# Kernel tuning notes

Hardware: AMD Instinct MI355X
Metric: run time of the kernel (lower is better)

Reference implementation:

```python
import jax, jax.numpy as jnp
import numpy as np

N = 4096
IN_DIM = 256
HID = 64
NHEADS = 4
OUT_DIM = 128
ALPHA = 0.5  # LeakyReLU negative slope
NEG_INF = -9e15


def gat_layer(x, mask, W, a, concat):
    """Dense GraphAttentionLayer (pyGAT style).
    x:[N,Fin], mask:[N,N] bool, W:[Fin,Fout], a:[2*Fout]."""
    Wh = x @ W                                   # [N, Fout]
    Fout = W.shape[1]
    f1 = Wh @ a[:Fout]                           # [N]
    f2 = Wh @ a[Fout:]                           # [N]
    e = jax.nn.leaky_relu(f1[:, None] + f2[None, :], negative_slope=ALPHA)  # [N,N]
    att = jax.nn.softmax(jnp.where(mask, e, NEG_INF), axis=1)               # [N,N]
    h = att @ Wh                                 # [N, Fout]
    return jax.nn.elu(h) if concat else h


def setup_inputs() -> dict:
    key = jax.random.key(0)
    ks = jax.random.split(key, 6)
    x = jax.random.normal(ks[0], (N, IN_DIM), dtype=jnp.float32)
    adj = jax.random.randint(ks[1], (N, N), 0, 2, dtype=jnp.int32)
    s_in = 1.0 / np.sqrt(IN_DIM)
    s_hid = 1.0 / np.sqrt(HID * NHEADS)
    W_heads = jax.random.uniform(ks[2], (NHEADS, IN_DIM, HID), jnp.float32, -s_in, s_in)
    a_heads = jax.random.uniform(ks[3], (NHEADS, 2 * HID), jnp.float32, -s_in, s_in)
    W_out = jax.random.uniform(ks[4], (HID * NHEADS, OUT_DIM), jnp.float32, -s_hid, s_hid)
    a_out = jax.random.uniform(ks[5], (2 * OUT_DIM,), jnp.float32, -s_hid, s_hid)
    return {"x": x, "adj": adj, "W_heads": W_heads, "a_heads": a_heads,
            "W_out": W_out, "a_out": a_out}


def reference(x, adj, W_heads, a_heads, W_out, a_out):
    mask = adj > 0
    # multi-head attention, concat along feature dim
    heads = jax.vmap(lambda W, a: gat_layer(x, mask, W, a, True))(W_heads, a_heads)
    h = jnp.transpose(heads, (1, 0, 2)).reshape(N, NHEADS * HID)  # [N, H*HID]
    # dropout=0 -> identity; final GAT layer (concat=False) + outer ELU
    out = jax.nn.elu(gat_layer(h, mask, W_out, a_out, False))     # [N, OUT_DIM]
    return out
```

## Files before the change

### kernel.cpp

```cpp
#include <hip/hip_runtime.h>
#include <hip/hip_bf16.h>

#define N 4096
#define IN_DIM 256
#define HID 64
#define NHEADS 4
#define OUT_DIM 128
#define LOG2E 1.44269504088896340736f

typedef __attribute__((ext_vector_type(8))) short bf16x8;
typedef __attribute__((ext_vector_type(4))) float f32x4;

__device__ __forceinline__ ushort2 bsplit(float v) {
    const ushort h = __hip_bfloat16_raw(__float2bfloat16(v)).x;
    const float vh = __uint_as_float((unsigned)h << 16);
    const ushort l = __hip_bfloat16_raw(__float2bfloat16(v - vh)).x;
    return make_ushort2(h, l);
}

__global__ __launch_bounds__(256, 4) void prep_kernel(
        const float* __restrict__ x, const float* __restrict__ W,
        const float* __restrict__ a, const int* __restrict__ adj,
        __hip_bfloat16* __restrict__ WhB,
        float* __restrict__ f1, float* __restrict__ f2,
        unsigned* __restrict__ maskT) {
    const int t = threadIdx.x;
    if (blockIdx.x < 256) {
        const int h = t >> 6, lane = t & 63, m = lane & 15, quad = lane >> 4;
        const int i0 = blockIdx.x * 16;
        const float* xrow = x + (size_t)(i0 + m) * IN_DIM;
        const float* Wp = W + (size_t)h * IN_DIM * HID;
        const f32x4 zero = {0.f, 0.f, 0.f, 0.f};
        f32x4 acc[4] = {zero, zero, zero, zero};
        for (int ks = 0; ks < 8; ks++) {
            const int kb = ks * 32 + quad * 8;
            const float4 xa = *(const float4*)(xrow + kb);
            const float4 xb = *(const float4*)(xrow + kb + 4);
            const float xf[8] = {xa.x, xa.y, xa.z, xa.w, xb.x, xb.y, xb.z, xb.w};
            bf16x8 xh, xl;
#pragma unroll
            for (int e = 0; e < 8; e++) {
                const ushort2 s = bsplit(xf[e]);
                xh[e] = (short)s.x; xl[e] = (short)s.y;
            }
#pragma unroll
            for (int ct = 0; ct < 4; ct++) {
                bf16x8 wh, wl;
#pragma unroll
                for (int e = 0; e < 8; e++) {
                    const ushort2 s =
                        bsplit(Wp[(size_t)(kb + e) * HID + ct * 16 + m]);
                    wh[e] = (short)s.x; wl[e] = (short)s.y;
                }
                acc[ct] = __builtin_amdgcn_mfma_f32_16x16x32_bf16(
                    xh, wh, acc[ct], 0, 0, 0);
                acc[ct] = __builtin_amdgcn_mfma_f32_16x16x32_bf16(
                    xl, wh, acc[ct], 0, 0, 0);
                acc[ct] = __builtin_amdgcn_mfma_f32_16x16x32_bf16(
                    xh, wl, acc[ct], 0, 0, 0);
            }
        }
        const int jblk = i0 >> 5, jb2 = (i0 >> 4) & 1;
#pragma unroll
        for (int ct = 0; ct < 4; ct++) {
#pragma unroll
            for (int r = 0; r < 4; r++) {
                const int jo = quad * 4 + r;
                const int lane_idx = m + 16 * (2 * jb2 + (jo >> 3));
                WhB[((((size_t)h * (N / 32) + jblk) * 4 + ct) * 64 + lane_idx) *
                        8 + (jo & 7)] = __float2bfloat16(acc[ct][r]);
            }
        }
        float av1[4], av2[4];
#pragma unroll
        for (int ct = 0; ct < 4; ct++) {
            av1[ct] = a[h * 2 * HID + ct * 16 + m];
            av2[ct] = a[h * 2 * HID + HID + ct * 16 + m];
        }
        float s1[4], s2[4];
#pragma unroll
        for (int r = 0; r < 4; r++) {
            s1[r] = 0.f; s2[r] = 0.f;
#pragma unroll
            for (int ct = 0; ct < 4; ct++) {
                s1[r] += acc[ct][r] * av1[ct];
                s2[r] += acc[ct][r] * av2[ct];
            }
        }
#pragma unroll
        for (int mm = 8; mm > 0; mm >>= 1) {
#pragma unroll
            for (int r = 0; r < 4; r++) {
                s1[r] += __shfl_xor(s1[r], mm, 64);
                s2[r] += __shfl_xor(s2[r], mm, 64);
            }
        }
        if (m == 0) {
#pragma unroll
            for (int r = 0; r < 4; r++) {
                f1[(size_t)h * N + i0 + quad * 4 + r] = s1[r] * LOG2E;
                f2[(size_t)h * N + i0 + quad * 4 + r] = s2[r] * LOG2E;
            }
        }
    } else {
        const int lane = t & 63, w = t >> 6;
        const int i = (blockIdx.x - 256) * 4 + w;
        const int4* arow = (const int4*)(adj + (size_t)i * N);
        for (int jb = 0; jb < N / 256; jb++) {
            const int4 a4 = arow[jb * 64 + lane];
            unsigned long long bal[4];
            bal[0] = __ballot(a4.x > 0);
            bal[1] = __ballot(a4.y > 0);
            bal[2] = __ballot(a4.z > 0);
            bal[3] = __ballot(a4.w > 0);
            if (lane < 8) {
                unsigned word = 0;
#pragma unroll
                for (int e = 0; e < 4; e++) {
                    unsigned xv = (unsigned)(bal[e] >> (8 * lane)) & 0xFFu;
                    xv = (xv | (xv << 12)) & 0x000F000Fu;
                    xv = (xv | (xv << 6))  & 0x03030303u;
                    xv = (xv | (xv << 3))  & 0x11111111u;
                    word |= xv << e;
                }
                maskT[(size_t)(jb * 8 + lane) * N + i] = word;
            }
        }
    }
}

template <int HEADS, int D, int DSL, int G, int MW, int OCC>
__global__ __launch_bounds__(G * 64, OCC) void attn_fused(
        const unsigned* __restrict__ maskT,
        const __hip_bfloat16* __restrict__ WhB,
        const float* __restrict__ f1g, const float* __restrict__ f2g,
        float* __restrict__ outp) {
    constexpr int CTtot = D / 16;
    constexpr int CTT = CTtot / DSL;
    constexpr int CC = (D == 64) ? 1 : 2;
    constexpr int KSTEPS = N / (32 * G);
    __shared__ float sh[MW * G * 16 * CC * 17];
    __shared__ float dsh[MW * G * 16];
    const int t = threadIdx.x;
    const int g = t >> 6, lane = t & 63;
    const int m = lane & 15, quad = lane >> 4;
    const int h = blockIdx.y / DSL, slc = blockIdx.y % DSL;
    const int i0 = blockIdx.x * (16 * MW);

    float f1v[MW];
#pragma unroll
    for (int mw = 0; mw < MW; mw++)
        f1v[mw] = f1g[(size_t)h * N + i0 + mw * 16 + m];

    const unsigned* mp = maskT + (size_t)(g * KSTEPS) * N + i0 + m;
    const float* fp = f2g + (size_t)h * N + g * (N / G) + quad * 8;
    const bf16x8* bp = (const bf16x8*)WhB +
                       ((size_t)h * (N / 32) * CTtot +
                        (size_t)(g * KSTEPS) * CTtot + slc * CTT) * 64 + lane;

    const f32x4 zero = {0.f, 0.f, 0.f, 0.f};
    f32x4 acc[MW][CTT];
    f32x4 sac[MW];
#pragma unroll
    for (int mw = 0; mw < MW; mw++) {
        sac[mw] = zero;
#pragma unroll
        for (int ct = 0; ct < CTT; ct++) acc[mw][ct] = zero;
    }
    const short one_bf = (short)0x3F80;
    const bf16x8 ones = {one_bf, one_bf, one_bf, one_bf,
                         one_bf, one_bf, one_bf, one_bf};

    unsigned mwrd[2][MW];
    float4 f2lo[2], f2hi[2];
    auto stage = [&](int b) {
#pragma unroll
        for (int mw = 0; mw < MW; mw++) mwrd[b][mw] = mp[mw * 16];
        f2lo[b] = *(const float4*)(fp);
        f2hi[b] = *(const float4*)(fp + 4);
    };

    stage(0); mp += N; fp += 32;
#pragma unroll 2
    for (int ks = 0; ks < KSTEPS; ks++) {
        const int cur = ks & 1;
        bf16x8 bfrag[CTT];
#pragma unroll
        for (int ct = 0; ct < CTT; ct++) bfrag[ct] = bp[ct * 64];
        bp += CTtot * 64;
        if (ks + 1 < KSTEPS) { stage(cur ^ 1); mp += N; fp += 32; }
        const float fe[8] = {f2lo[cur].x, f2lo[cur].y, f2lo[cur].z, f2lo[cur].w,
                             f2hi[cur].x, f2hi[cur].y, f2hi[cur].z, f2hi[cur].w};
        bf16x8 afr[MW];
#pragma unroll
        for (int mw = 0; mw < MW; mw++) {
            const unsigned mword = (mwrd[cur][mw] >> (quad * 8)) & 0xFFu;
            const unsigned spread = mword * 0x8001u;
            float p[8];
#pragma unroll
            for (int e = 0; e < 8; e++) {
                const float tt = f1v[mw] + fe[e];
                const float lr = fmaxf(tt, 0.5f * tt);
                p[e] = __builtin_amdgcn_exp2f(lr);
            }
            union { bf16x8 v; unsigned u32[4]; __hip_bfloat162 h2[4]; } u;
#pragma unroll
            for (int e2 = 0; e2 < 4; e2++) {
                u.h2[e2] = __float22bfloat162_rn(
                    make_float2(p[2 * e2], p[2 * e2 + 1]));
                const unsigned mk =
                    ((spread >> (2 * e2)) & 0x00010001u) * 0xFFFFu;
                u.u32[e2] &= mk;
            }
            afr[mw] = u.v;
        }
#pragma unroll
        for (int ct = 0; ct < CTT; ct++)
#pragma unroll
            for (int mw = 0; mw < MW; mw++)
                acc[mw][ct] = __builtin_amdgcn_mfma_f32_16x16x32_bf16(
                    afr[mw], bfrag[ct], acc[mw][ct], 0, 0, 0);
#pragma unroll
        for (int mw = 0; mw < MW; mw++)
            sac[mw] = __builtin_amdgcn_mfma_f32_16x16x32_bf16(
                afr[mw], ones, sac[mw], 0, 0, 0);
    }

#pragma unroll
    for (int rd = 0; rd < CTT / CC; rd++) {
#pragma unroll
        for (int mw = 0; mw < MW; mw++) {
#pragma unroll
            for (int cc = 0; cc < CC; cc++) {
#pragma unroll
                for (int r = 0; r < 4; r++)
                    sh[(((mw * G + g) * 16 + quad * 4 + r) * CC + cc) * 17 + m] =
                        acc[mw][rd * CC + cc][r];
            }
            if (rd == 0 && m == 0) {
#pragma unroll
                for (int r = 0; r < 4; r++)
                    dsh[(mw * G + g) * 16 + quad * 4 + r] = sac[mw][r];
            }
        }
        __syncthreads();
        if (t < 16 * CC * 16) {
            int row, chl;
            if (D == 64) { row = t & 15; chl = (t >> 4) & 15; }
            else         { chl = t & 31; row = (t >> 5) & 15; }
#pragma unroll
            for (int mw = 0; mw < MW; mw++) {
                float av = 0.f, ss = 0.f;
#pragma unroll
                for (int gg = 0; gg < G; gg++) {
                    av += sh[(((mw * G + gg) * 16 + row) * CC + (chl >> 4)) * 17 +
                             (chl & 15)];
                    ss += dsh[(mw * G + gg) * 16 + row];
                }
                float v = av / ss;
                v = (v > 0.f) ? v : (__builtin_amdgcn_exp2f(v * LOG2E) - 1.f);
                const int chg = h * D + slc * (CTT * 16) + rd * CC * 16 + chl;
                const int irow = i0 + mw * 16 + row;
                if (D == 64)
                    outp[(size_t)irow * (NHEADS * HID) + chg] = v;
                else
                    outp[(size_t)irow * D + chg] = v;
            }
        }
        __syncthreads();
    }
}

__global__ __launch_bounds__(512, 2) void gemm2_kernel(
        const float* __restrict__ h1, const float* __restrict__ W2,
        const float* __restrict__ a2, __hip_bfloat16* __restrict__ WhB2,
        float* __restrict__ f1, float* __restrict__ f2) {
    __shared__ float fred[8][16][2];
    const int t = threadIdx.x;
    const int w = t >> 6, lane = t & 63, m = lane & 15, quad = lane >> 4;
    const int i0 = blockIdx.x * 16;
    const float* arow = h1 + (size_t)(i0 + m) * IN_DIM;
    const float* wp = W2 + w * 16 + m;
    const f32x4 zero = {0.f, 0.f, 0.f, 0.f};
    f32x4 acc = zero;
    for (int ks = 0; ks < 8; ks++) {
        const int kb = ks * 32 + quad * 8;
        const float4 xa = *(const float4*)(arow + kb);
        const float4 xb = *(const float4*)(arow + kb + 4);
        const float xf[8] = {xa.x, xa.y, xa.z, xa.w, xb.x, xb.y, xb.z, xb.w};
        bf16x8 xh, xl, wh, wl;
#pragma unroll
        for (int e = 0; e < 8; e++) {
            const ushort2 s = bsplit(xf[e]);
            xh[e] = (short)s.x; xl[e] = (short)s.y;
        }
#pragma unroll
        for (int e = 0; e < 8; e++) {
            const ushort2 s = bsplit(wp[(size_t)(kb + e) * OUT_DIM]);
            wh[e] = (short)s.x; wl[e] = (short)s.y;
        }
        acc = __builtin_amdgcn_mfma_f32_16x16x32_bf16(xh, wh, acc, 0, 0, 0);
        acc = __builtin_amdgcn_mfma_f32_16x16x32_bf16(xl, wh, acc, 0, 0, 0);
        acc = __builtin_amdgcn_mfma_f32_16x16x32_bf16(xh, wl, acc, 0, 0, 0);
    }
    const int jblk = i0 >> 5, jb2 = (i0 >> 4) & 1;
#pragma unroll
    for (int r = 0; r < 4; r++) {
        const int jo = quad * 4 + r;
        const int lane_idx = m + 16 * (2 * jb2 + (jo >> 3));
        WhB2[(((size_t)jblk * 8 + w) * 64 + lane_idx) * 8 + (jo & 7)] =
            __float2bfloat16(acc[r]);
    }
    const float av1 = a2[w * 16 + m], av2 = a2[OUT_DIM + w * 16 + m];
    float s1[4], s2[4];
#pragma unroll
    for (int r = 0; r < 4; r++) { s1[r] = acc[r] * av1; s2[r] = acc[r] * av2; }
#pragma unroll
    for (int mm = 8; mm > 0; mm >>= 1) {
#pragma unroll
        for (int r = 0; r < 4; r++) {
            s1[r] += __shfl_xor(s1[r], mm, 64);
            s2[r] += __shfl_xor(s2[r], mm, 64);
        }
    }
    if (m == 0) {
#pragma unroll
        for (int r = 0; r < 4; r++) {
            fred[w][quad * 4 + r][0] = s1[r];
            fred[w][quad * 4 + r][1] = s2[r];
        }
    }
    __syncthreads();
    if (t < 32) {
        const int row = t & 15, fn = t >> 4;
        float s = 0.f;
#pragma unroll
        for (int w8 = 0; w8 < 8; w8++) s += fred[w8][row][fn];
        (fn ? f2 : f1)[i0 + row] = s * LOG2E;
    }
}

extern "C" void kernel_launch(void* const* d_in, const int* in_sizes, int n_in,
                              void* d_out, int out_size, void* d_ws, size_t ws_size,
                              hipStream_t stream) {
    const float* x   = (const float*)d_in[0];
    const int*   adj = (const int*)d_in[1];
    const float* Wh_ = (const float*)d_in[2];
    const float* ah  = (const float*)d_in[3];
    const float* W2  = (const float*)d_in[4];
    const float* a2  = (const float*)d_in[5];
    float* out = (float*)d_out;

    float* ws = (float*)d_ws;
    float* f1a = ws;
    float* f2a = f1a + (size_t)NHEADS * N;
    float* f1b = f2a + (size_t)NHEADS * N;
    float* f2b = f1b + N;
    float* h1  = f2b + N;
    __hip_bfloat16* WhB1 = (__hip_bfloat16*)(h1 + (size_t)IN_DIM * N);
    __hip_bfloat16* WhB2 = WhB1 + (size_t)NHEADS * HID * N;
    unsigned* maskT = (unsigned*)(WhB2 + (size_t)OUT_DIM * N);

    prep_kernel<<<1280, 256, 0, stream>>>(x, Wh_, ah, adj, WhB1, f1a, f2a, maskT);
    attn_fused<NHEADS, HID, 1, 8, 1, 8>
        <<<dim3(N / 16, NHEADS), 512, 0, stream>>>(maskT, WhB1, f1a, f2a, h1);
    gemm2_kernel<<<N / 16, 512, 0, stream>>>(h1, W2, a2, WhB2, f1b, f2b);
    attn_fused<1, OUT_DIM, 1, 16, 1, 4>
        <<<dim3(N / 16, 1), 1024, 0, stream>>>(maskT, WhB2, f1b, f2b, out);
}
```

Before: 191.1 us.

## Factor exp of leaky-relu scores into per-node products, retune attention launches

```diff
diff --git a/kernel.cpp b/kernel.cpp
--- a/kernel.cpp
+++ b/kernel.cpp
@@ -22,7 +22,8 @@
         const float* __restrict__ x, const float* __restrict__ W,
         const float* __restrict__ a, const int* __restrict__ adj,
         __hip_bfloat16* __restrict__ WhB,
-        float* __restrict__ f1, float* __restrict__ f2,
+        float* __restrict__ E1, float* __restrict__ S1,
+        float* __restrict__ E2, float* __restrict__ S2,
         unsigned* __restrict__ maskT) {
     const int t = threadIdx.x;
     if (blockIdx.x < 256) {
@@ -98,8 +99,11 @@
         if (m == 0) {
 #pragma unroll
             for (int r = 0; r < 4; r++) {
-                f1[(size_t)h * N + i0 + quad * 4 + r] = s1[r] * LOG2E;
-                f2[(size_t)h * N + i0 + quad * 4 + r] = s2[r] * LOG2E;
+                const size_t ix = (size_t)h * N + i0 + quad * 4 + r;
+                E1[ix] = __builtin_amdgcn_exp2f(s1[r] * LOG2E);
+                S1[ix] = __builtin_amdgcn_exp2f(s1[r] * (0.5f * LOG2E));
+                E2[ix] = __builtin_amdgcn_exp2f(s2[r] * LOG2E);
+                S2[ix] = __builtin_amdgcn_exp2f(s2[r] * (0.5f * LOG2E));
             }
         }
     } else {
@@ -133,7 +137,8 @@
 __global__ __launch_bounds__(G * 64, OCC) void attn_fused(
         const unsigned* __restrict__ maskT,
         const __hip_bfloat16* __restrict__ WhB,
-        const float* __restrict__ f1g, const float* __restrict__ f2g,
+        const float* __restrict__ E1g, const float* __restrict__ S1g,
+        const float* __restrict__ E2g, const float* __restrict__ S2g,
         float* __restrict__ outp) {
     constexpr int CTtot = D / 16;
     constexpr int CTT = CTtot / DSL;
@@ -147,13 +152,16 @@
     const int h = blockIdx.y / DSL, slc = blockIdx.y % DSL;
     const int i0 = blockIdx.x * (16 * MW);
 
-    float f1v[MW];
-#pragma unroll
-    for (int mw = 0; mw < MW; mw++)
-        f1v[mw] = f1g[(size_t)h * N + i0 + mw * 16 + m];
+    float e1v[MW], s1v[MW];
+#pragma unroll
+    for (int mw = 0; mw < MW; mw++) {
+        e1v[mw] = E1g[(size_t)h * N + i0 + mw * 16 + m];
+        s1v[mw] = S1g[(size_t)h * N + i0 + mw * 16 + m];
+    }
 
     const unsigned* mp = maskT + (size_t)(g * KSTEPS) * N + i0 + m;
-    const float* fp = f2g + (size_t)h * N + g * (N / G) + quad * 8;
+    const float* ep = E2g + (size_t)h * N + g * (N / G) + quad * 8;
+    const float* sp = S2g + (size_t)h * N + g * (N / G) + quad * 8;
     const bf16x8* bp = (const bf16x8*)WhB +
                        ((size_t)h * (N / 32) * CTtot +
                         (size_t)(g * KSTEPS) * CTtot + slc * CTT) * 64 + lane;
@@ -172,15 +180,17 @@
                          one_bf, one_bf, one_bf, one_bf};
 
     unsigned mwrd[2][MW];
-    float4 f2lo[2], f2hi[2];
+    float4 e2lo[2], e2hi[2], s2lo[2], s2hi[2];
     auto stage = [&](int b) {
 #pragma unroll
         for (int mw = 0; mw < MW; mw++) mwrd[b][mw] = mp[mw * 16];
-        f2lo[b] = *(const float4*)(fp);
-        f2hi[b] = *(const float4*)(fp + 4);
+        e2lo[b] = *(const float4*)(ep);
+        e2hi[b] = *(const float4*)(ep + 4);
+        s2lo[b] = *(const float4*)(sp);
+        s2hi[b] = *(const float4*)(sp + 4);
     };
 
-    stage(0); mp += N; fp += 32;
+    stage(0); mp += N; ep += 32; sp += 32;
 #pragma unroll 2
     for (int ks = 0; ks < KSTEPS; ks++) {
         const int cur = ks & 1;
@@ -188,9 +198,11 @@
 #pragma unroll
         for (int ct = 0; ct < CTT; ct++) bfrag[ct] = bp[ct * 64];
         bp += CTtot * 64;
-        if (ks + 1 < KSTEPS) { stage(cur ^ 1); mp += N; fp += 32; }
-        const float fe[8] = {f2lo[cur].x, f2lo[cur].y, f2lo[cur].z, f2lo[cur].w,
-                             f2hi[cur].x, f2hi[cur].y, f2hi[cur].z, f2hi[cur].w};
+        if (ks + 1 < KSTEPS) { stage(cur ^ 1); mp += N; ep += 32; sp += 32; }
+        const float Ee[8] = {e2lo[cur].x, e2lo[cur].y, e2lo[cur].z, e2lo[cur].w,
+                             e2hi[cur].x, e2hi[cur].y, e2hi[cur].z, e2hi[cur].w};
+        const float Se[8] = {s2lo[cur].x, s2lo[cur].y, s2lo[cur].z, s2lo[cur].w,
+                             s2hi[cur].x, s2hi[cur].y, s2hi[cur].z, s2hi[cur].w};
         bf16x8 afr[MW];
 #pragma unroll
         for (int mw = 0; mw < MW; mw++) {
@@ -198,11 +210,8 @@
             const unsigned spread = mword * 0x8001u;
             float p[8];
 #pragma unroll
-            for (int e = 0; e < 8; e++) {
-                const float tt = f1v[mw] + fe[e];
-                const float lr = fmaxf(tt, 0.5f * tt);
-                p[e] = __builtin_amdgcn_exp2f(lr);
-            }
+            for (int e = 0; e < 8; e++)
+                p[e] = fmaxf(e1v[mw] * Ee[e], s1v[mw] * Se[e]);
             union { bf16x8 v; unsigned u32[4]; __hip_bfloat162 h2[4]; } u;
 #pragma unroll
             for (int e2 = 0; e2 < 4; e2++) {
@@ -274,7 +283,8 @@
 __global__ __launch_bounds__(512, 2) void gemm2_kernel(
         const float* __restrict__ h1, const float* __restrict__ W2,
         const float* __restrict__ a2, __hip_bfloat16* __restrict__ WhB2,
-        float* __restrict__ f1, float* __restrict__ f2) {
+        float* __restrict__ E1, float* __restrict__ S1,
+        float* __restrict__ E2, float* __restrict__ S2) {
     __shared__ float fred[8][16][2];
     const int t = threadIdx.x;
     const int w = t >> 6, lane = t & 63, m = lane & 15, quad = lane >> 4;
@@ -336,7 +346,10 @@
         float s = 0.f;
 #pragma unroll
         for (int w8 = 0; w8 < 8; w8++) s += fred[w8][row][fn];
-        (fn ? f2 : f1)[i0 + row] = s * LOG2E;
+        const float e = __builtin_amdgcn_exp2f(s * LOG2E);
+        const float sq = __builtin_amdgcn_exp2f(s * (0.5f * LOG2E));
+        if (fn) { E2[i0 + row] = e; S2[i0 + row] = sq; }
+        else    { E1[i0 + row] = e; S1[i0 + row] = sq; }
     }
 }
 
@@ -352,19 +365,27 @@
     float* out = (float*)d_out;
 
     float* ws = (float*)d_ws;
-    float* f1a = ws;
-    float* f2a = f1a + (size_t)NHEADS * N;
-    float* f1b = f2a + (size_t)NHEADS * N;
-    float* f2b = f1b + N;
-    float* h1  = f2b + N;
+    float* E1a = ws;
+    float* S1a = E1a + (size_t)NHEADS * N;
+    float* E2a = S1a + (size_t)NHEADS * N;
+    float* S2a = E2a + (size_t)NHEADS * N;
+    float* E1b = S2a + (size_t)NHEADS * N;
+    float* S1b = E1b + N;
+    float* E2b = S1b + N;
+    float* S2b = E2b + N;
+    float* h1  = S2b + N;
     __hip_bfloat16* WhB1 = (__hip_bfloat16*)(h1 + (size_t)IN_DIM * N);
     __hip_bfloat16* WhB2 = WhB1 + (size_t)NHEADS * HID * N;
     unsigned* maskT = (unsigned*)(WhB2 + (size_t)OUT_DIM * N);
 
-    prep_kernel<<<1280, 256, 0, stream>>>(x, Wh_, ah, adj, WhB1, f1a, f2a, maskT);
-    attn_fused<NHEADS, HID, 1, 8, 1, 8>
-        <<<dim3(N / 16, NHEADS), 512, 0, stream>>>(maskT, WhB1, f1a, f2a, h1);
-    gemm2_kernel<<<N / 16, 512, 0, stream>>>(h1, W2, a2, WhB2, f1b, f2b);
-    attn_fused<1, OUT_DIM, 1, 16, 1, 4>
-        <<<dim3(N / 16, 1), 1024, 0, stream>>>(maskT, WhB2, f1b, f2b, out);
-}
+    prep_kernel<<<1280, 256, 0, stream>>>(x, Wh_, ah, adj, WhB1,
+                                          E1a, S1a, E2a, S2a, maskT);
+    attn_fused<NHEADS, HID, 1, 8, 2, 2>
+        <<<dim3(N / 32, NHEADS), 512, 0, stream>>>(maskT, WhB1,
+                                                   E1a, S1a, E2a, S2a, h1);
+    gemm2_kernel<<<N / 16, 512, 0, stream>>>(h1, W2, a2, WhB2,
+                                             E1b, S1b, E2b, S2b);
+    attn_fused<1, OUT_DIM, 1, 8, 1, 2>
+        <<<dim3(N / 16, 1), 512, 0, stream>>>(maskT, WhB2,
+                                              E1b, S1b, E2b, S2b, out);
+}
```

Measured after the change: 168.7 us. 11.7% less time.
